# Kernel tuning notes

Hardware: AMD Instinct MI355X
Metric: run time of the kernel (lower is better)

The kernel has to match this reference:

```python
import jax, jax.numpy as jnp
import numpy as np

B, N, F_NUM, H_NUM = 2, 8192, 64, 64


def _linear_params(key, fan_in, fan_out, bias=True):
    k1, k2 = jax.random.split(key)
    bound = 1.0 / np.sqrt(fan_in)
    W = jax.random.uniform(k1, (fan_in, fan_out), minval=-bound, maxval=bound, dtype=jnp.float32)
    if bias:
        b = jax.random.uniform(k2, (fan_out,), minval=-bound, maxval=bound, dtype=jnp.float32)
        return W, b
    return W


def setup_inputs() -> dict:
    key = jax.random.key(0)
    ks = jax.random.split(key, 12)
    Wk, bk = _linear_params(ks[0], F_NUM, H_NUM)
    Wa, ba = _linear_params(ks[1], H_NUM, F_NUM)
    Wq = _linear_params(ks[2], H_NUM, H_NUM, bias=False)
    Wks = _linear_params(ks[3], H_NUM, H_NUM, bias=False)
    Wv = _linear_params(ks[4], H_NUM, H_NUM, bias=False)
    Wp1, bp1 = _linear_params(ks[5], 4, H_NUM)
    Wp2, bp2 = _linear_params(ks[6], H_NUM, H_NUM)
    Wt1, bt1 = _linear_params(ks[7], H_NUM, H_NUM)
    Wt2, bt2 = _linear_params(ks[8], H_NUM, H_NUM)
    xyzp = jax.random.normal(ks[9], (B, N, 4), dtype=jnp.float32)
    features = jax.random.normal(ks[10], (B, N, F_NUM), dtype=jnp.float32)
    return dict(xyzp=xyzp, features=features, Wk=Wk, bk=bk, Wq=Wq, Wks=Wks, Wv=Wv,
                Wp1=Wp1, bp1=bp1, Wp2=Wp2, bp2=bp2, Wt1=Wt1, bt1=bt1, Wt2=Wt2, bt2=bt2,
                Wa=Wa, ba=ba, k_nearest=16)


def _knn_idx(xyz, K):
    sq = jnp.sum(xyz * xyz, axis=-1)                      # [B,N]
    d = sq[:, :, None] + sq[:, None, :] - 2.0 * jnp.einsum('bnd,bmd->bnm', xyz, xyz)
    _, idx = jax.lax.top_k(-d, K)                         # [B,N,K] nearest (incl. self)
    return idx


def _knn_gather(x, idx):
    # x: [B,N,C], idx: [B,N,K] -> [B,N,K,C]
    return jax.vmap(lambda xb, ib: xb[ib])(x, idx)


def reference(xyzp, features, Wk, bk, Wq, Wks, Wv, Wp1, bp1, Wp2, bp2,
              Wt1, bt1, Wt2, bt2, Wa, ba, k_nearest):
    xyz = xyzp[:, :, :3]
    idx = _knn_idx(xyz, k_nearest)                        # [B,N,K]
    # positional encoding MLP on relative xyzp
    rel = xyzp[:, :, None, :] - _knn_gather(xyzp, idx)    # [B,N,K,4]
    pos_enc = jax.nn.relu(rel @ Wp1 + bp1) @ Wp2 + bp2    # [B,N,K,H]
    x = features @ Wk + bk                                # [B,N,H]
    q = x @ Wq                                            # [B,N,H]
    k = _knn_gather(x @ Wks, idx)                         # [B,N,K,H]
    v = _knn_gather(x @ Wv, idx)                          # [B,N,K,H]
    a_in = q[:, :, None, :] - k + pos_enc                 # [B,N,K,H]
    attn = jax.nn.relu(a_in @ Wt1 + bt1) @ Wt2 + bt2      # [B,N,K,H]
    attn = jax.nn.softmax(attn / np.sqrt(H_NUM).astype(np.float32), axis=-2)
    res = jnp.einsum('bnkh,bnkh->bnh', attn, v + pos_enc) # per-channel weighted sum over K
    return res @ Wa + ba + features
```

## Files before the change

kernel.cpp:

```cpp
#include <hip/hip_runtime.h>

#define NPTS 8192
#define HDIM 64
#define KNN 16
#define LOG2E 1.4426950408889634f

typedef __attribute__((ext_vector_type(8))) short bf8_t;
typedef __attribute__((ext_vector_type(4))) float f4_t;
#define MFMA16(a, b, c) __builtin_amdgcn_mfma_f32_16x16x32_bf16(a, b, c, 0, 0, 0)

__device__ __forceinline__ float fast_exp(float x) {
    float y = x * LOG2E;
    float r;
    asm volatile("v_exp_f32 %0, %1\n\ts_nop 1" : "=v"(r) : "v"(y));
    return r;
}
__device__ __forceinline__ unsigned short f2b(float x) {
    unsigned v = __float_as_uint(x);
    return (unsigned short)((v + 0x7FFFu + ((v >> 16) & 1u)) >> 16);
}

#define OFF_QW   0u
#define OFF_KW   (4u << 20)
#define OFF_VW   (8u << 20)
#define OFF_FRAG (12u << 20)
#define OFF_KNN  ((12u << 20) + 32768u)

__global__ void prefrag_kernel(const float* __restrict__ Wp2,
                               const float* __restrict__ Wt1,
                               const float* __restrict__ Wt2,
                               unsigned short* __restrict__ dst)
{
    int i = blockIdx.x * 256 + threadIdx.x;
    if (i >= 3 * 4096) return;
    int st = i >> 12, e = i & 4095;
    const float* W = (st == 0) ? Wp2 : (st == 1) ? Wt1 : Wt2;
    int k = e >> 6, n = e & 63;
    int s = k >> 5, quad = (k >> 3) & 3, j = k & 7;
    int t = n >> 4, l = quad * 16 + (n & 15);
    dst[st * 4096 + (s * 4 + t) * 512 + l * 8 + j] = f2b(W[e]);
}

__global__ __launch_bounds__(1024) void proj_kernel(
    const float* __restrict__ feat,
    const float* __restrict__ Wk, const float* __restrict__ bk,
    const float* __restrict__ Wq, const float* __restrict__ Wks,
    const float* __restrict__ Wv,
    float* __restrict__ qw, float* __restrict__ kw, float* __restrict__ vw)
{
    __shared__ __align__(16) float4 sW[4][1024];
    int tid = threadIdx.x;
    sW[0][tid] = ((const float4*)Wk)[tid];
    sW[1][tid] = ((const float4*)Wq)[tid];
    sW[2][tid] = ((const float4*)Wks)[tid];
    sW[3][tid] = ((const float4*)Wv)[tid];
    __syncthreads();
    const float* sWk  = (const float*)sW[0];
    const float* sWq  = (const float*)sW[1];
    const float* sWks = (const float*)sW[2];
    const float* sWv  = (const float*)sW[3];

    int w = tid >> 6, lane = tid & 63;
    int p = blockIdx.x * 16 + w;
    float f = feat[(size_t)p * HDIM + lane];
    float x = bk[lane];
    #pragma unroll 8
    for (int c = 0; c < 64; ++c) x += __shfl(f, c) * sWk[c * 64 + lane];
    float q = 0.f, k = 0.f, v = 0.f;
    #pragma unroll 8
    for (int c = 0; c < 64; ++c) {
        float xc = __shfl(x, c);
        q += xc * sWq[c * 64 + lane];
        k += xc * sWks[c * 64 + lane];
        v += xc * sWv[c * 64 + lane];
    }
    qw[(size_t)p * HDIM + lane] = q;
    kw[(size_t)p * HDIM + lane] = k;
    vw[(size_t)p * HDIM + lane] = v;
}

__global__ __launch_bounds__(256) void knn2_kernel(
    const float* __restrict__ xyzp, int* __restrict__ knnIdx)
{
    int w = threadIdx.x >> 6, lane = threadIdx.x & 63;
    int wid = blockIdx.x * 4 + w;
    int pbase = wid * 2;
    int b = pbase >> 13;
    int nbase = pbase & (NPTS - 1);
    const float4* xb4 = (const float4*)xyzp + (size_t)b * NPTS;

    float qx[2], qy[2], qz[2], qs[2];
    #pragma unroll
    for (int qi = 0; qi < 2; ++qi) {
        float4 s = xb4[nbase + qi];
        qx[qi] = s.x; qy[qi] = s.y; qz[qi] = s.z;
        qs[qi] = s.x * s.x + s.y * s.y + s.z * s.z;
    }

    float dh[2][4]; int ih[2][4];
    #pragma unroll
    for (int qi = 0; qi < 2; ++qi)
        #pragma unroll
        for (int j = 0; j < 4; ++j) { dh[qi][j] = 3.4e38f; ih[qi][j] = 0x7fffffff; }

    float tau[2];
    tau[0] = 3.4e38f; tau[1] = 3.4e38f;

    #pragma unroll 1
    for (int t = 0; t < NPTS / 256; ++t) {
        float4 c[4];
        #pragma unroll
        for (int u = 0; u < 4; ++u)
            c[u] = xb4[(t * 4 + u) * 64 + lane];
        #pragma unroll
        for (int u = 0; u < 4; ++u) {
            int m = (t * 4 + u) * 64 + lane;
            float cs = c[u].x * c[u].x + c[u].y * c[u].y + c[u].z * c[u].z;
            #pragma unroll
            for (int qi = 0; qi < 2; ++qi) {
                float d = qs[qi] + cs
                        - 2.0f * (qx[qi] * c[u].x + qy[qi] * c[u].y + qz[qi] * c[u].z);
                if (__any(d <= tau[qi])) {
                    bool c3 = d < dh[qi][3];
                    bool c2 = d < dh[qi][2];
                    bool c1 = d < dh[qi][1];
                    bool c0 = d < dh[qi][0];
                    dh[qi][3] = c2 ? dh[qi][2] : (c3 ? d : dh[qi][3]);
                    ih[qi][3] = c2 ? ih[qi][2] : (c3 ? m : ih[qi][3]);
                    dh[qi][2] = c1 ? dh[qi][1] : (c2 ? d : dh[qi][2]);
                    ih[qi][2] = c1 ? ih[qi][1] : (c2 ? m : ih[qi][2]);
                    dh[qi][1] = c0 ? dh[qi][0] : (c1 ? d : dh[qi][1]);
                    ih[qi][1] = c0 ? ih[qi][0] : (c1 ? m : ih[qi][1]);
                    dh[qi][0] = c0 ? d : dh[qi][0];
                    ih[qi][0] = c0 ? m : ih[qi][0];
                }
            }
        }
        if (t & 1) {
            #pragma unroll
            for (int qi = 0; qi < 2; ++qi) {
                float t4 = dh[qi][3];
                t4 = fminf(t4, __shfl_xor(t4, 1));
                t4 = fminf(t4, __shfl_xor(t4, 2));
                t4 = fminf(t4, __shfl_xor(t4, 4));
                t4 = fminf(t4, __shfl_xor(t4, 8));
                t4 = fmaxf(t4, __shfl_xor(t4, 16));
                t4 = fmaxf(t4, __shfl_xor(t4, 32));
                tau[qi] = t4;
            }
        }
    }

    #pragma unroll
    for (int qi = 0; qi < 2; ++qi) {
        int mynb = 0, head = 0;
        #pragma unroll 1
        for (int r = 0; r < KNN; ++r) {
            float d = dh[qi][0]; int i = ih[qi][0];
            #pragma unroll
            for (int s = 1; s < 64; s <<= 1) {
                float d2 = __shfl_xor(d, s); int i2 = __shfl_xor(i, s);
                if (d2 < d || (d2 == d && i2 < i)) { d = d2; i = i2; }
            }
            if (lane == r) mynb = i;
            if (ih[qi][0] == i) {
                dh[qi][0] = dh[qi][1]; ih[qi][0] = ih[qi][1];
                dh[qi][1] = dh[qi][2]; ih[qi][1] = ih[qi][2];
                dh[qi][2] = dh[qi][3]; ih[qi][2] = ih[qi][3];
                dh[qi][3] = 3.4e38f; ih[qi][3] = 0x7fffffff;
                ++head;
            }
        }
        if (__any(head >= 4)) {
            float eh[16]; int ei[16];
            #pragma unroll
            for (int j = 0; j < 16; ++j) { eh[j] = 3.4e38f; ei[j] = 0x7fffffff; }
            for (int t = 0; t < NPTS / 64; ++t) {
                int m = t * 64 + lane;
                float4 c4 = xb4[m];
                float cs = c4.x * c4.x + c4.y * c4.y + c4.z * c4.z;
                float d = qs[qi] + cs
                        - 2.0f * (qx[qi] * c4.x + qy[qi] * c4.y + qz[qi] * c4.z);
                if (d < eh[15]) {
                    eh[15] = d; ei[15] = m;
                    #pragma unroll
                    for (int j = 15; j >= 1; --j)
                        if (eh[j] < eh[j - 1]) {
                            float td = eh[j]; eh[j] = eh[j - 1]; eh[j - 1] = td;
                            int ti = ei[j]; ei[j] = ei[j - 1]; ei[j - 1] = ti;
                        }
                }
            }
            #pragma unroll 1
            for (int r = 0; r < KNN; ++r) {
                float d = eh[0]; int i = ei[0];
                #pragma unroll
                for (int s = 1; s < 64; s <<= 1) {
                    float d2 = __shfl_xor(d, s); int i2 = __shfl_xor(i, s);
                    if (d2 < d || (d2 == d && i2 < i)) { d = d2; i = i2; }
                }
                if (lane == r) mynb = i;
                if (ei[0] == i) {
                    #pragma unroll
                    for (int j = 0; j < 15; ++j) { eh[j] = eh[j + 1]; ei[j] = ei[j + 1]; }
                    eh[15] = 3.4e38f; ei[15] = 0x7fffffff;
                }
            }
        }
        mynb = min(max(mynb, 0), NPTS - 1);
        if (lane < KNN) knnIdx[(size_t)(pbase + qi) * KNN + lane] = mynb;
    }
}

__global__ __launch_bounds__(256) void LocalTransformer_80513456931527_kernel(
    const float* __restrict__ xyzp, const float* __restrict__ features,
    const float* __restrict__ Wp1,  const float* __restrict__ bp1,
    const float* __restrict__ bp2,  const float* __restrict__ bt1,
    const float* __restrict__ bt2,
    const float* __restrict__ Wa,   const float* __restrict__ ba,
    const float* __restrict__ qw, const float* __restrict__ kw,
    const float* __restrict__ vw,
    const unsigned short* __restrict__ fragw,
    const int* __restrict__ knnIdx,
    float* __restrict__ out)
{
    __shared__ __align__(16) float sBounce[4][16 * 68 + 4];

    int tid = threadIdx.x, w = tid >> 6, lane = tid & 63;
    int p = blockIdx.x * 4 + w;
    int b = p >> 13;
    float* bb = sBounce[w];

    int quad = lane >> 4, l15 = lane & 15;
    int mynb = knnIdx[(size_t)p * KNN + l15];
    mynb = min(max(mynb, 0), NPTS - 1);
    int nb_a = mynb;
    int nbm[4];
    #pragma unroll
    for (int r = 0; r < 4; ++r) nbm[r] = __shfl(mynb, quad * 4 + r);

    const float4 xq4 = *(const float4*)(xyzp + (size_t)p * 4);
    const float4 xn4 = *(const float4*)(xyzp + ((size_t)b * NPTS + nb_a) * 4);
    float rel0 = xq4.x - xn4.x, rel1 = xq4.y - xn4.y;
    float rel2 = xq4.z - xn4.z, rel3 = xq4.w - xn4.w;

    bf8_t pe1f[2];
    #pragma unroll
    for (int s = 0; s < 2; ++s) {
        int hb = s * 32 + quad * 8;
        float W0[8], W1[8], W2[8], W3[8], Bb[8];
        *(float4*)&W0[0] = *(const float4*)(Wp1 +       hb);
        *(float4*)&W0[4] = *(const float4*)(Wp1 +       hb + 4);
        *(float4*)&W1[0] = *(const float4*)(Wp1 +  64 + hb);
        *(float4*)&W1[4] = *(const float4*)(Wp1 +  64 + hb + 4);
        *(float4*)&W2[0] = *(const float4*)(Wp1 + 128 + hb);
        *(float4*)&W2[4] = *(const float4*)(Wp1 + 128 + hb + 4);
        *(float4*)&W3[0] = *(const float4*)(Wp1 + 192 + hb);
        *(float4*)&W3[4] = *(const float4*)(Wp1 + 192 + hb + 4);
        *(float4*)&Bb[0] = *(const float4*)(bp1 + hb);
        *(float4*)&Bb[4] = *(const float4*)(bp1 + hb + 4);
        #pragma unroll
        for (int j = 0; j < 8; ++j) {
            float a = Bb[j] + rel0 * W0[j] + rel1 * W1[j]
                            + rel2 * W2[j] + rel3 * W3[j];
            pe1f[s][j] = (short)f2b(fmaxf(a, 0.f));
        }
    }

    const bf8_t* BW = (const bf8_t*)fragw;
    f4_t pe2c[4];
    #pragma unroll
    for (int t = 0; t < 4; ++t) {
        f4_t acc = {0.f, 0.f, 0.f, 0.f};
        acc = MFMA16(pe1f[0], BW[0 * 512 + (0 * 4 + t) * 64 + lane], acc);
        acc = MFMA16(pe1f[1], BW[0 * 512 + (1 * 4 + t) * 64 + lane], acc);
        float bias = bp2[t * 16 + l15];
        #pragma unroll
        for (int r = 0; r < 4; ++r) acc[r] += bias;
        pe2c[t] = acc;
    }

    f4_t ainc[4], vpec[4];
    #pragma unroll
    for (int t = 0; t < 4; ++t) {
        float qv = qw[(size_t)p * HDIM + t * 16 + l15];
        #pragma unroll
        for (int r = 0; r < 4; ++r) {
            size_t nbo = ((size_t)b * NPTS + nbm[r]) * HDIM + t * 16 + l15;
            ainc[t][r] = qv - kw[nbo] + pe2c[t][r];
            vpec[t][r] = vw[nbo] + pe2c[t][r];
        }
    }

    #pragma unroll
    for (int t = 0; t < 4; ++t)
        #pragma unroll
        for (int r = 0; r < 4; ++r)
            bb[(quad * 4 + r) * 68 + t * 16 + l15] = ainc[t][r];
    asm volatile("s_waitcnt lgkmcnt(0)" ::: "memory");
    bf8_t af[2];
    #pragma unroll
    for (int s = 0; s < 2; ++s) {
        float tmp[8];
        *(float4*)&tmp[0] = *(const float4*)&bb[l15 * 68 + s * 32 + quad * 8];
        *(float4*)&tmp[4] = *(const float4*)&bb[l15 * 68 + s * 32 + quad * 8 + 4];
        #pragma unroll
        for (int j = 0; j < 8; ++j) af[s][j] = (short)f2b(tmp[j]);
    }

    f4_t t1c[4];
    #pragma unroll
    for (int t = 0; t < 4; ++t) {
        f4_t acc = {0.f, 0.f, 0.f, 0.f};
        acc = MFMA16(af[0], BW[1 * 512 + (0 * 4 + t) * 64 + lane], acc);
        acc = MFMA16(af[1], BW[1 * 512 + (1 * 4 + t) * 64 + lane], acc);
        float bias = bt1[t * 16 + l15];
        #pragma unroll
        for (int r = 0; r < 4; ++r) t1c[t][r] = fmaxf(acc[r] + bias, 0.f);
    }

    asm volatile("s_waitcnt lgkmcnt(0)" ::: "memory");
    #pragma unroll
    for (int t = 0; t < 4; ++t)
        #pragma unroll
        for (int r = 0; r < 4; ++r)
            bb[(quad * 4 + r) * 68 + t * 16 + l15] = t1c[t][r];
    asm volatile("s_waitcnt lgkmcnt(0)" ::: "memory");
    bf8_t tf[2];
    #pragma unroll
    for (int s = 0; s < 2; ++s) {
        float tmp[8];
        *(float4*)&tmp[0] = *(const float4*)&bb[l15 * 68 + s * 32 + quad * 8];
        *(float4*)&tmp[4] = *(const float4*)&bb[l15 * 68 + s * 32 + quad * 8 + 4];
        #pragma unroll
        for (int j = 0; j < 8; ++j) tf[s][j] = (short)f2b(tmp[j]);
    }

    f4_t lgc[4];
    #pragma unroll
    for (int t = 0; t < 4; ++t) {
        f4_t acc = {0.f, 0.f, 0.f, 0.f};
        acc = MFMA16(tf[0], BW[2 * 512 + (0 * 4 + t) * 64 + lane], acc);
        acc = MFMA16(tf[1], BW[2 * 512 + (1 * 4 + t) * 64 + lane], acc);
        float bias = bt2[t * 16 + l15];
        #pragma unroll
        for (int r = 0; r < 4; ++r) lgc[t][r] = (acc[r] + bias) * 0.125f;
    }

    float res[4];
    #pragma unroll
    for (int t = 0; t < 4; ++t) {
        float m0 = fmaxf(fmaxf(lgc[t][0], lgc[t][1]), fmaxf(lgc[t][2], lgc[t][3]));
        m0 = fmaxf(m0, __shfl_xor(m0, 16));
        m0 = fmaxf(m0, __shfl_xor(m0, 32));
        float e0 = fast_exp(lgc[t][0] - m0), e1 = fast_exp(lgc[t][1] - m0);
        float e2 = fast_exp(lgc[t][2] - m0), e3 = fast_exp(lgc[t][3] - m0);
        float sl = e0 + e1 + e2 + e3;
        float rl = e0 * vpec[t][0] + e1 * vpec[t][1]
                 + e2 * vpec[t][2] + e3 * vpec[t][3];
        sl += __shfl_xor(sl, 16); sl += __shfl_xor(sl, 32);
        rl += __shfl_xor(rl, 16); rl += __shfl_xor(rl, 32);
        res[t] = rl / sl;
    }

    float rh = (quad == 0) ? res[0] : (quad == 1) ? res[1]
             : (quad == 2) ? res[2] : res[3];
    float f = features[(size_t)p * HDIM + lane];
    float o = ba[lane];
    #pragma unroll 8
    for (int c = 0; c < 64; ++c) o += __shfl(rh, c) * Wa[c * 64 + lane];
    out[(size_t)p * HDIM + lane] = o + f;
}

extern "C" void kernel_launch(void* const* d_in, const int* in_sizes, int n_in,
                              void* d_out, int out_size, void* d_ws, size_t ws_size,
                              hipStream_t stream)
{
    (void)in_sizes; (void)n_in; (void)out_size; (void)ws_size;
    const float* xyzp     = (const float*)d_in[0];
    const float* features = (const float*)d_in[1];
    const float* Wk  = (const float*)d_in[2];
    const float* bk  = (const float*)d_in[3];
    const float* Wq  = (const float*)d_in[4];
    const float* Wks = (const float*)d_in[5];
    const float* Wv  = (const float*)d_in[6];
    const float* Wp1 = (const float*)d_in[7];
    const float* bp1 = (const float*)d_in[8];
    const float* Wp2 = (const float*)d_in[9];
    const float* bp2 = (const float*)d_in[10];
    const float* Wt1 = (const float*)d_in[11];
    const float* bt1 = (const float*)d_in[12];
    const float* Wt2 = (const float*)d_in[13];
    const float* bt2 = (const float*)d_in[14];
    const float* Wa  = (const float*)d_in[15];
    const float* ba  = (const float*)d_in[16];
    float* out = (float*)d_out;
    char* ws = (char*)d_ws;

    float* qw = (float*)(ws + OFF_QW);
    float* kw = (float*)(ws + OFF_KW);
    float* vw = (float*)(ws + OFF_VW);
    unsigned short* fragw = (unsigned short*)(ws + OFF_FRAG);
    int* knnIdx = (int*)(ws + OFF_KNN);

    prefrag_kernel<<<48, 256, 0, stream>>>(Wp2, Wt1, Wt2, fragw);
    proj_kernel<<<(2 * NPTS) / 16, 1024, 0, stream>>>(
        features, Wk, bk, Wq, Wks, Wv, qw, kw, vw);
    knn2_kernel<<<(2 * NPTS) / 8, 256, 0, stream>>>(xyzp, knnIdx);
    LocalTransformer_80513456931527_kernel<<<(2 * NPTS) / 4, 256, 0, stream>>>(
        xyzp, features, Wp1, bp1, bp2, bt1, bt2, Wa, ba,
        qw, kw, vw, fragw, knnIdx, out);
}
```

Baseline: 354.5 us.

## Merge prefrag, projection and KNN kernels into one heterogeneous launch

Three preprocessing kernels become a single launch in which block ranges are dispatched by index: weight fragment conversion, QKV projection (two blocks per triple), and KNN search (one block per triple). The interleaving lets the compute-light projection blocks run alongside the long KNN blocks and removes two launch gaps. The projection now reads its weights straight from global memory instead of staging them in LDS, and it uses 256-thread blocks where it used 1024 before.

```diff
diff --git a/kernel.cpp b/kernel.cpp
--- a/kernel.cpp
+++ b/kernel.cpp
@@ -26,64 +26,62 @@
 #define OFF_FRAG (12u << 20)
 #define OFF_KNN  ((12u << 20) + 32768u)
 
-__global__ void prefrag_kernel(const float* __restrict__ Wp2,
-                               const float* __restrict__ Wt1,
-                               const float* __restrict__ Wt2,
-                               unsigned short* __restrict__ dst)
-{
-    int i = blockIdx.x * 256 + threadIdx.x;
-    if (i >= 3 * 4096) return;
-    int st = i >> 12, e = i & 4095;
-    const float* W = (st == 0) ? Wp2 : (st == 1) ? Wt1 : Wt2;
-    int k = e >> 6, n = e & 63;
-    int s = k >> 5, quad = (k >> 3) & 3, j = k & 7;
-    int t = n >> 4, l = quad * 16 + (n & 15);
-    dst[st * 4096 + (s * 4 + t) * 512 + l * 8 + j] = f2b(W[e]);
-}
-
-__global__ __launch_bounds__(1024) void proj_kernel(
+#define KNN_BLOCKS 2048
+#define PROJ_BLOCKS 4096
+#define PRE_BLOCKS 48
+
+__global__ __launch_bounds__(256) void fused_pre_kernel(
+    const float* __restrict__ xyzp,
     const float* __restrict__ feat,
     const float* __restrict__ Wk, const float* __restrict__ bk,
     const float* __restrict__ Wq, const float* __restrict__ Wks,
     const float* __restrict__ Wv,
-    float* __restrict__ qw, float* __restrict__ kw, float* __restrict__ vw)
+    const float* __restrict__ Wp2, const float* __restrict__ Wt1,
+    const float* __restrict__ Wt2,
+    float* __restrict__ qw, float* __restrict__ kw, float* __restrict__ vw,
+    unsigned short* __restrict__ fragw,
+    int* __restrict__ knnIdx)
 {
-    __shared__ __align__(16) float4 sW[4][1024];
-    int tid = threadIdx.x;
-    sW[0][tid] = ((const float4*)Wk)[tid];
-    sW[1][tid] = ((const float4*)Wq)[tid];
-    sW[2][tid] = ((const float4*)Wks)[tid];
-    sW[3][tid] = ((const float4*)Wv)[tid];
-    __syncthreads();
-    const float* sWk  = (const float*)sW[0];
-    const float* sWq  = (const float*)sW[1];
-    const float* sWks = (const float*)sW[2];
-    const float* sWv  = (const float*)sW[3];
-
-    int w = tid >> 6, lane = tid & 63;
-    int p = blockIdx.x * 16 + w;
-    float f = feat[(size_t)p * HDIM + lane];
-    float x = bk[lane];
-    #pragma unroll 8
-    for (int c = 0; c < 64; ++c) x += __shfl(f, c) * sWk[c * 64 + lane];
-    float q = 0.f, k = 0.f, v = 0.f;
-    #pragma unroll 8
-    for (int c = 0; c < 64; ++c) {
-        float xc = __shfl(x, c);
-        q += xc * sWq[c * 64 + lane];
-        k += xc * sWks[c * 64 + lane];
-        v += xc * sWv[c * 64 + lane];
-    }
-    qw[(size_t)p * HDIM + lane] = q;
-    kw[(size_t)p * HDIM + lane] = k;
-    vw[(size_t)p * HDIM + lane] = v;
-}
-
-__global__ __launch_bounds__(256) void knn2_kernel(
-    const float* __restrict__ xyzp, int* __restrict__ knnIdx)
-{
+    int bid = blockIdx.x;
+
+    if (bid < PRE_BLOCKS) {
+        int i = bid * 256 + threadIdx.x;
+        if (i >= 3 * 4096) return;
+        int st = i >> 12, e = i & 4095;
+        const float* W = (st == 0) ? Wp2 : (st == 1) ? Wt1 : Wt2;
+        int k = e >> 6, n = e & 63;
+        int s = k >> 5, quad = (k >> 3) & 3, j = k & 7;
+        int t = n >> 4, l = quad * 16 + (n & 15);
+        fragw[st * 4096 + (s * 4 + t) * 512 + l * 8 + j] = f2b(W[e]);
+        return;
+    }
+
+    int j3 = bid - PRE_BLOCKS;
+    int triple = j3 / 3, pos = j3 - triple * 3;
     int w = threadIdx.x >> 6, lane = threadIdx.x & 63;
-    int wid = blockIdx.x * 4 + w;
+
+    if (pos != 0) {
+        int pb = triple * 2 + (pos - 1);
+        int p = pb * 4 + w;
+        float f = feat[(size_t)p * HDIM + lane];
+        float x = bk[lane];
+        #pragma unroll 8
+        for (int c = 0; c < 64; ++c) x += __shfl(f, c) * Wk[c * 64 + lane];
+        float q = 0.f, k = 0.f, v = 0.f;
+        #pragma unroll 8
+        for (int c = 0; c < 64; ++c) {
+            float xc = __shfl(x, c);
+            q += xc * Wq[c * 64 + lane];
+            k += xc * Wks[c * 64 + lane];
+            v += xc * Wv[c * 64 + lane];
+        }
+        qw[(size_t)p * HDIM + lane] = q;
+        kw[(size_t)p * HDIM + lane] = k;
+        vw[(size_t)p * HDIM + lane] = v;
+        return;
+    }
+
+    int wid = triple * 4 + w;
     int pbase = wid * 2;
     int b = pbase >> 13;
     int nbase = pbase & (NPTS - 1);
@@ -403,10 +401,9 @@
     unsigned short* fragw = (unsigned short*)(ws + OFF_FRAG);
     int* knnIdx = (int*)(ws + OFF_KNN);
 
-    prefrag_kernel<<<48, 256, 0, stream>>>(Wp2, Wt1, Wt2, fragw);
-    proj_kernel<<<(2 * NPTS) / 16, 1024, 0, stream>>>(
-        features, Wk, bk, Wq, Wks, Wv, qw, kw, vw);
-    knn2_kernel<<<(2 * NPTS) / 8, 256, 0, stream>>>(xyzp, knnIdx);
+    fused_pre_kernel<<<PRE_BLOCKS + 3 * KNN_BLOCKS, 256, 0, stream>>>(
+        xyzp, features, Wk, bk, Wq, Wks, Wv, Wp2, Wt1, Wt2,
+        qw, kw, vw, fragw, knnIdx);
     LocalTransformer_80513456931527_kernel<<<(2 * NPTS) / 4, 256, 0, stream>>>(
         xyzp, features, Wp1, bp1, bp2, bt1, bt2, Wa, ba,
         qw, kw, vw, fragw, knnIdx, out);
```

Result: faster. 335.7 us (-5.3%).
